# Kernel tuning notes

Measured on AMD Instinct MI355X. Metric: run time of the kernel, lower is better.

The kernel has to match this reference:

```python
import jax, jax.numpy as jnp
import numpy as np

N_ENT = 50000
N_USR = 10000
N_NODES = N_ENT + N_USR
D = 64            # entity_dim
AE_H = [128, 32]  # autoencoder hidden dims
CONV = [32, 16]   # graph conv output dims
R = 16            # n_relations
E = 1920000       # n_edges (avg degree 32)
B = 4096          # scoring batch


def setup_inputs() -> dict:
    key = jax.random.key(0)
    ks = jax.random.split(key, 24)
    s = 0.05
    rn = lambda k, shp: jax.random.normal(k, shp, jnp.float32) * s
    inp = {
        # int graph / batch inputs
        "users": jax.random.randint(ks[0], (B,), 0, N_USR),
        "items": jax.random.randint(ks[1], (B,), 0, N_ENT),
        "edge_src": jax.random.randint(ks[2], (E,), 0, N_NODES),
        "edge_dst": jax.random.randint(ks[3], (E,), 0, N_NODES),
        "edge_rel": jax.random.randint(ks[4], (E,), 0, R),
        # embeddings
        "entity_emb": rn(ks[5], (N_ENT, D)),
        "user_emb": rn(ks[6], (N_USR, D)),
        # autoencoder (weights stored [in, out])
        "enc_W0": rn(ks[7], (D, AE_H[0])), "enc_b0": jnp.zeros((AE_H[0],), jnp.float32),
        "enc_W1": rn(ks[8], (AE_H[0], AE_H[1])), "enc_b1": jnp.zeros((AE_H[1],), jnp.float32),
        "dec_W0": rn(ks[9], (AE_H[1], AE_H[0])), "dec_b0": jnp.zeros((AE_H[0],), jnp.float32),
        "dec_W1": rn(ks[10], (AE_H[0], D)), "dec_b1": jnp.zeros((D,), jnp.float32),
        # conv layer 1: input_dim=32 -> W_r [R, 64, 32], linear [64 -> 32]
        "Wr1": rn(ks[11], (R, 2 * CONV[0], CONV[0])),
        "lin_W1": rn(ks[12], (2 * CONV[0], CONV[0])), "lin_b1": jnp.zeros((CONV[0],), jnp.float32),
        # conv layer 2: input_dim=32 -> W_r [R, 64, 32], linear [64 -> 16]
        "Wr2": rn(ks[13], (R, 2 * CONV[0], CONV[0])),
        "lin_W2": rn(ks[14], (2 * CONV[0], CONV[1])), "lin_b2": jnp.zeros((CONV[1],), jnp.float32),
    }
    return inp


def _graph_conv(x, edge_src, edge_dst, edge_rel, W_r, lin_W, lin_b):
    # gate logit = sum_j (concat(h_dst, h_src) @ W_r[rel])_j
    #            = concat(h_dst, h_src) . W_r[rel].sum(-1)  (exact identity)
    w_sum = W_r.sum(axis=-1)                      # [R, 2*in]
    h_dst = x[edge_dst]                            # [E, in]
    h_src = x[edge_src]                            # [E, in]
    c = jnp.concatenate([h_dst, h_src], axis=-1)   # [E, 2*in]
    gate = jax.nn.sigmoid(jnp.sum(c * w_sum[edge_rel], axis=-1, keepdims=True))  # [E,1]
    weighted = h_src * gate                        # [E, in]
    n = x.shape[0]
    agg_sum = jax.ops.segment_sum(weighted, edge_dst, num_segments=n)           # [N, in]
    cnt = jax.ops.segment_sum(jnp.ones((edge_dst.shape[0], 1), x.dtype), edge_dst, num_segments=n)
    agg = jnp.where(cnt > 0, agg_sum / jnp.maximum(cnt, 1.0), 0.0)              # scatter-mean
    combined = jnp.concatenate([x, agg], axis=-1)  # [N, 2*in]
    return jax.nn.leaky_relu(combined @ lin_W + lin_b, negative_slope=0.01)


def reference(entity_emb, user_emb,
              enc_W0, enc_b0, enc_W1, enc_b1,
              dec_W0, dec_b0, dec_W1, dec_b1,
              Wr1, lin_W1, lin_b1, Wr2, lin_W2, lin_b2,
              users, items, edge_src, edge_dst, edge_rel):
    all_emb = jnp.concatenate([entity_emb, user_emb], axis=0)  # [N, 64]
    # autoencoder: ReLU between layers, none at the end of encode/decode
    encoded = jax.nn.relu(all_emb @ enc_W0 + enc_b0) @ enc_W1 + enc_b1  # [N, 32]
    decoded = jax.nn.relu(encoded @ dec_W0 + dec_b0) @ dec_W1 + dec_b1  # [N, 64]
    ae_loss = jnp.mean((decoded - all_emb) ** 2)

    x1 = _graph_conv(encoded, edge_src, edge_dst, edge_rel, Wr1, lin_W1, lin_b1)  # [N, 32]
    x2 = _graph_conv(x1, edge_src, edge_dst, edge_rel, Wr2, lin_W2, lin_b2)       # [N, 16]
    final = jnp.concatenate([x1, x2], axis=-1)  # [N, 48]

    user_nodes = N_ENT + users
    scores = jnp.sum(final[user_nodes] * final[items], axis=-1)  # [B]
    return scores, ae_loss
```

## Files before the change

### kernel.cpp

```cpp
#include <hip/hip_runtime.h>
#include <hip/hip_fp16.h>
#include <math.h>

#define N_ENT 50000
#define N_USR 10000
#define NN    60000
#define DD    64
#define H0    128
#define ENCD  32
#define RR    16
#define NB    256
#define BSH   8
#define NBU   235

__device__ __forceinline__ float4 ld4(const float* p){ return *reinterpret_cast<const float4*>(p); }
__device__ __forceinline__ void st4(float* p, float4 v){ *reinterpret_cast<float4*>(p) = v; }

__global__ __launch_bounds__(512, 6) void k_ae_hist(const float* __restrict__ ent, const float* __restrict__ usr,
    const float* __restrict__ eW0, const float* __restrict__ eb0,
    const float* __restrict__ eW1, const float* __restrict__ eb1,
    const float* __restrict__ dW0c, const float* __restrict__ db0,
    const float* __restrict__ dW1c, const float* __restrict__ db1,
    float* __restrict__ enc, float* __restrict__ loss_out,
    const int* __restrict__ edst, int* __restrict__ bktCnt,
    const float* __restrict__ Wr1, const float* __restrict__ Wr2, float* __restrict__ wsum,
    int E_, int nbAE, int nbTh){
  __shared__ float hs[H0][65];
  __shared__ float es[ENCD][65];
  __shared__ float sred[8];
  int bid = blockIdx.x;
  int t = threadIdx.x;

  if (bid >= nbAE){
    int rb = bid - nbAE;
    if (rb < nbTh){
      int* hh = (int*)&hs[0][0];
      if (t < NB) hh[t] = 0;
      __syncthreads();
      int i0 = rb*8192;
      #pragma unroll
      for (int k=0;k<16;k++){
        int e = i0 + k*512 + t;
        if (e < E_) atomicAdd(&hh[((unsigned)edst[e])>>BSH], 1);
      }
      __syncthreads();
      if (t < NB){ int c = hh[t]; if (c) atomicAdd(&bktCnt[t], c); }
    } else {
      int i = (rb - nbTh)*512 + t;
      if (i < 2*RR*DD){
        const float* Wr = (i < RR*DD) ? Wr1 : Wr2;
        int loc = i & (RR*DD - 1);
        const float* p = Wr + (size_t)loc*32;
        float s = 0.f;
        #pragma unroll
        for (int k=0;k<32;k++) s += p[k];
        wsum[i] = s;
      }
    }
    return;
  }

  int nl = t & 63;
  int wid = __builtin_amdgcn_readfirstlane(t >> 6);
  int gnode = bid*64 + nl;
  bool valid = gnode < NN;
  const float* xr = valid ? ((gnode < N_ENT) ? ent + (size_t)gnode*DD
                                             : usr + (size_t)(gnode-N_ENT)*DD)
                          : ent;

  {
    int j0 = wid*16;
    float acc[16];
    #pragma unroll
    for (int k=0;k<16;k++) acc[k]=eb0[j0+k];
    #pragma unroll
    for (int dc=0; dc<DD; dc+=16){
      float xv[16];
      #pragma unroll
      for (int q=0;q<4;q++){
        float4 v = ld4(xr + dc + 4*q);
        xv[4*q]=v.x; xv[4*q+1]=v.y; xv[4*q+2]=v.z; xv[4*q+3]=v.w;
      }
      #pragma unroll
      for (int dd=0; dd<16; dd++){
        const float* w = eW0 + (size_t)(dc+dd)*H0 + j0;
        #pragma unroll
        for (int k=0;k<16;k++) acc[k]=fmaf(xv[dd], w[k], acc[k]);
      }
    }
    #pragma unroll
    for (int k=0;k<16;k++) hs[j0+k][nl]=fmaxf(acc[k],0.f);
  }
  __syncthreads();

  {
    int k0 = wid*4;
    float acc[4];
    #pragma unroll
    for (int k=0;k<4;k++) acc[k]=eb1[k0+k];
    #pragma unroll 4
    for (int j=0;j<H0;j++){
      float hv = hs[j][nl];
      const float* w = eW1 + (size_t)j*ENCD + k0;
      #pragma unroll
      for (int k=0;k<4;k++) acc[k]=fmaf(hv,w[k],acc[k]);
    }
    #pragma unroll
    for (int k=0;k<4;k++) es[k0+k][nl]=acc[k];
  }
  __syncthreads();

  {
    int n2 = t >> 3;
    int k2 = (t & 7) * 4;
    int gn2 = bid*64 + n2;
    if (gn2 < NN){
      float4 a;
      a.x=es[k2+0][n2]; a.y=es[k2+1][n2]; a.z=es[k2+2][n2]; a.w=es[k2+3][n2];
      st4(enc + (size_t)gn2*ENCD + k2, a);
    }
  }

  {
    int j0 = wid*16;
    float acc[16];
    #pragma unroll
    for (int k=0;k<16;k++) acc[k]=db0[j0+k];
    #pragma unroll 4
    for (int d=0;d<ENCD;d++){
      float x = es[d][nl];
      const float* w = dW0c + (size_t)d*H0 + j0;
      #pragma unroll
      for (int k=0;k<16;k++) acc[k]=fmaf(x,w[k],acc[k]);
    }
    #pragma unroll
    for (int k=0;k<16;k++) hs[j0+k][nl]=fmaxf(acc[k],0.f);
  }
  __syncthreads();

  float part = 0.f;
  {
    int c0 = wid*8;
    float acc[8];
    #pragma unroll
    for (int k=0;k<8;k++) acc[k]=db1[c0+k];
    #pragma unroll 4
    for (int j=0;j<H0;j++){
      float hv = hs[j][nl];
      const float* w = dW1c + (size_t)j*DD + c0;
      #pragma unroll
      for (int k=0;k<8;k++) acc[k]=fmaf(hv,w[k],acc[k]);
    }
    if (valid){
      float xl[8];
      float4 v0 = ld4(xr + c0), v1 = ld4(xr + c0 + 4);
      xl[0]=v0.x; xl[1]=v0.y; xl[2]=v0.z; xl[3]=v0.w;
      xl[4]=v1.x; xl[5]=v1.y; xl[6]=v1.z; xl[7]=v1.w;
      #pragma unroll
      for (int k=0;k<8;k++){ float d_ = acc[k]-xl[k]; part = fmaf(d_,d_,part); }
    }
  }
  #pragma unroll
  for (int off=32; off>0; off>>=1) part += __shfl_down(part, off, 64);
  if ((t&63)==0) sred[wid] = part;
  __syncthreads();
  if (t==0){
    float s = 0.f;
    #pragma unroll
    for (int k=0;k<8;k++) s += sred[k];
    atomicAdd(loss_out, s * (1.0f/((float)NN*(float)DD)));
  }
}

__global__ __launch_bounds__(256) void k_scan256(const int* __restrict__ bktCnt, int* __restrict__ bktBase){
  __shared__ int wps[4];
  int t = threadIdx.x;
  int v = bktCnt[t];
  int x = v;
  #pragma unroll
  for (int off=1; off<64; off<<=1){
    int y = __shfl_up(x, off, 64);
    if ((t & 63) >= off) x += y;
  }
  if ((t & 63) == 63) wps[t >> 6] = x;
  __syncthreads();
  if (t < 4){
    int wv = wps[t];
    int wx = wv;
    #pragma unroll
    for (int off=1; off<4; off<<=1){
      int y = __shfl_up(wx, off, 4);
      if (t >= off) wx += y;
    }
    wps[t] = wx - wv;
  }
  __syncthreads();
  bktBase[t] = (x - v) + wps[t >> 6];
}

__global__ __launch_bounds__(256) void k_bucketA(const int* __restrict__ esrc, const int* __restrict__ edst,
    const int* __restrict__ erel, const int* __restrict__ bktBase, int* __restrict__ bktFill,
    unsigned* __restrict__ bktData, int E_){
  __shared__ int h[NB];
  __shared__ int gbase[NB];
  h[threadIdx.x]=0;
  __syncthreads();
  int i0 = blockIdx.x*4096;
  int dcache[16];
  #pragma unroll
  for (int k=0;k<16;k++){
    int e = i0 + k*256 + threadIdx.x;
    int d = (e < E_) ? edst[e] : -1;
    dcache[k] = d;
    if (d >= 0) atomicAdd(&h[((unsigned)d)>>BSH], 1);
  }
  __syncthreads();
  {
    int c = h[threadIdx.x];
    int off = c ? atomicAdd(&bktFill[threadIdx.x], c) : 0;
    gbase[threadIdx.x] = bktBase[threadIdx.x] + off;
    h[threadIdx.x] = 0;
  }
  __syncthreads();
  #pragma unroll
  for (int k=0;k<16;k++){
    int e = i0 + k*256 + threadIdx.x;
    if (e >= E_) continue;
    int d = dcache[k];
    int b = ((unsigned)d) >> BSH;
    int slot = atomicAdd(&h[b], 1);
    unsigned rec = (unsigned)esrc[e] | ((unsigned)erel[e] << 16) | ((unsigned)(d & 0xFF) << 20);
    bktData[(size_t)gbase[b] + slot] = rec;
  }
}

__global__ __launch_bounds__(256) void k_buildB(const unsigned* __restrict__ bktData,
    const int* __restrict__ bktBase, const int* __restrict__ bktCnt,
    int* __restrict__ rowp, int* __restrict__ packed){
  __shared__ int cnt[NB];
  __shared__ int start[NB];
  __shared__ int wps[4];
  int b = blockIdx.x;
  int base = bktBase[b];
  int n = bktCnt[b];
  int t = threadIdx.x;
  cnt[t] = 0;
  __syncthreads();
  for (int i=t; i<n; i+=256) atomicAdd(&cnt[(bktData[base+i] >> 20) & 0xFF], 1);
  __syncthreads();
  int v = cnt[t];
  cnt[t] = 0;
  int x = v;
  #pragma unroll
  for (int off=1; off<64; off<<=1){
    int y = __shfl_up(x, off, 64);
    if ((t & 63) >= off) x += y;
  }
  if ((t & 63) == 63) wps[t >> 6] = x;
  __syncthreads();
  if (t < 4){
    int wv = wps[t];
    int wx = wv;
    #pragma unroll
    for (int off=1; off<4; off<<=1){
      int y = __shfl_up(wx, off, 4);
      if (t >= off) wx += y;
    }
    wps[t] = wx - wv;
  }
  __syncthreads();
  int sv = (x - v) + wps[t >> 6];
  start[t] = sv;
  int node = (b << BSH) + t;
  if (node <= NN) rowp[node] = base + sv;
  __syncthreads();
  for (int i=t; i<n; i+=256){
    unsigned r = bktData[base+i];
    int dl = (r >> 20) & 0xFF;
    int p = start[dl] + atomicAdd(&cnt[dl], 1);
    packed[base + p] = (int)r;
  }
}

__global__ __launch_bounds__(256) void k_dots(const float* __restrict__ x, const float* __restrict__ wsum,
    float* __restrict__ dA, __half* __restrict__ dbrec, __half* __restrict__ xrec){
  __shared__ float wl[RR*DD];
  for (int i = threadIdx.x; i < RR*DD; i += 256){
    int r = i & 15; int j = i >> 4;
    wl[i] = wsum[r*DD + j];
  }
  __syncthreads();
  int t = blockIdx.x*256 + threadIdx.x;
  if (t >= NN*RR) return;
  int n = t >> 4, r = t & 15;
  const float* xr = x + (size_t)n*ENCD;
  float a = 0.f, b = 0.f;
  float xlo = 0.f, xhi = 0.f;
  #pragma unroll
  for (int q=0;q<8;q++){
    float4 v = ld4(xr + 4*q);
    int j = 4*q;
    if (r >= j && r < j+4){ float tmp[4]={v.x,v.y,v.z,v.w}; xlo = tmp[r-j]; }
    if (r+16 >= j && r+16 < j+4){ float tmp[4]={v.x,v.y,v.z,v.w}; xhi = tmp[r+16-j]; }
    a = fmaf(v.x, wl[(j+0)*16 + r], a);
    a = fmaf(v.y, wl[(j+1)*16 + r], a);
    a = fmaf(v.z, wl[(j+2)*16 + r], a);
    a = fmaf(v.w, wl[(j+3)*16 + r], a);
    b = fmaf(v.x, wl[(32+j+0)*16 + r], b);
    b = fmaf(v.y, wl[(32+j+1)*16 + r], b);
    b = fmaf(v.z, wl[(32+j+2)*16 + r], b);
    b = fmaf(v.w, wl[(32+j+3)*16 + r], b);
  }
  dA[t] = a;
  dbrec[t] = __float2half(b);
  xrec[(size_t)n*32 + r]      = __float2half(xlo);
  xrec[(size_t)n*32 + 16 + r] = __float2half(xhi);
}

__global__ __launch_bounds__(256) void k_gates(const int* __restrict__ packed,
    const int* __restrict__ bktBase, const int* __restrict__ bktCnt,
    const float* __restrict__ dA, const __half* __restrict__ dbrec, __half* __restrict__ gat){
  int b = blockIdx.x >> 2, g = blockIdx.x & 3;
  int base = bktBase[b], n = bktCnt[b];
  int lo = (n*g) >> 2, hi = (n*(g+1)) >> 2;
  for (int i = lo + (int)threadIdx.x; i < hi; i += 256){
    int p = packed[base+i];
    int s = p & 0xFFFF;
    int r = (p >> 16) & 15;
    int dl = (p >> 20) & 0xFF;
    int dst = (b << BSH) | dl;
    float z = dA[dst*16 + r] + __half2float(dbrec[s*16 + r]);
    gat[base+i] = __float2half(1.f/(1.f + __expf(-z)));
  }
}

__global__ __launch_bounds__(256) void k_agg(const __half2* __restrict__ xrec2, const int* __restrict__ packed,
    const __half* __restrict__ gat, const int* __restrict__ rowp, float* __restrict__ agg){
  int node = blockIdx.x*8 + (threadIdx.x >> 5);
  int l = threadIdx.x & 31;
  int half = l >> 4;
  int l16 = l & 15;
  if (node >= NN) return;
  int beg = rowp[node], end = rowp[node+1];
  float ax = 0.f, ay = 0.f;
  #pragma unroll 2
  for (int i = beg + half; i < end; i += 2){
    int p = packed[i];
    int s = p & 0xFFFF;
    float g = __half2float(gat[i]);
    float2 fx = __half22float2(xrec2[(size_t)s*16 + l16]);
    ax = fmaf(fx.x, g, ax);
    ay = fmaf(fx.y, g, ay);
  }
  ax += __shfl_xor(ax, 16, 32);
  ay += __shfl_xor(ay, 16, 32);
  if (half == 0){
    int deg = end - beg;
    float inv = (deg > 0) ? 1.f/(float)deg : 0.f;
    float2 o; o.x = ax*inv; o.y = ay*inv;
    *reinterpret_cast<float2*>(&agg[(size_t)node*ENCD + 2*l16]) = o;
  }
}

__global__ __launch_bounds__(256) void k_lin(const float* __restrict__ x, const float* __restrict__ agg,
    const float* __restrict__ W, const float* __restrict__ b, float* __restrict__ out, int outd){
  int n = blockIdx.x*256 + threadIdx.x;
  if (n >= NN) return;
  int k0 = blockIdx.y * 16;
  const float* xr = x   + (size_t)n*ENCD;
  const float* ar = agg + (size_t)n*ENCD;
  float xv[32], av[32];
  #pragma unroll
  for (int q=0;q<8;q++){ float4 v = ld4(xr+4*q); xv[4*q]=v.x; xv[4*q+1]=v.y; xv[4*q+2]=v.z; xv[4*q+3]=v.w; }
  #pragma unroll
  for (int q=0;q<8;q++){ float4 v = ld4(ar+4*q); av[4*q]=v.x; av[4*q+1]=v.y; av[4*q+2]=v.z; av[4*q+3]=v.w; }
  float acc[16];
  #pragma unroll
  for (int t=0;t<16;t++) acc[t] = b[k0+t];
  #pragma unroll
  for (int j=0;j<32;j++){
    #pragma unroll
    for (int t=0;t<16;t++) acc[t] = fmaf(xv[j], W[(size_t)j*outd + k0 + t], acc[t]);
  }
  #pragma unroll
  for (int j=0;j<32;j++){
    #pragma unroll
    for (int t=0;t<16;t++) acc[t] = fmaf(av[j], W[(size_t)(32+j)*outd + k0 + t], acc[t]);
  }
  float* o = out + (size_t)n*outd + k0;
  #pragma unroll
  for (int q=0;q<4;q++){
    float4 v;
    float a0=acc[4*q],a1=acc[4*q+1],a2=acc[4*q+2],a3=acc[4*q+3];
    v.x = a0>0.f? a0 : 0.01f*a0;
    v.y = a1>0.f? a1 : 0.01f*a1;
    v.z = a2>0.f? a2 : 0.01f*a2;
    v.w = a3>0.f? a3 : 0.01f*a3;
    st4(o + 4*q, v);
  }
}

__global__ __launch_bounds__(256) void k_score(const float* __restrict__ x1, const float* __restrict__ x2,
    const int* __restrict__ users, const int* __restrict__ items, float* __restrict__ out, int Bn){
  int b = blockIdx.x*256 + threadIdx.x;
  if (b >= Bn) return;
  int u  = N_ENT + users[b];
  int it = items[b];
  const float* a1 = x1 + (size_t)u*32;
  const float* c1 = x1 + (size_t)it*32;
  const float* a2 = x2 + (size_t)u*16;
  const float* c2 = x2 + (size_t)it*16;
  float s = 0.f;
  #pragma unroll
  for (int q=0;q<8;q++){
    float4 va=ld4(a1+4*q), vb=ld4(c1+4*q);
    s = fmaf(va.x,vb.x,s); s = fmaf(va.y,vb.y,s); s = fmaf(va.z,vb.z,s); s = fmaf(va.w,vb.w,s);
  }
  #pragma unroll
  for (int q=0;q<4;q++){
    float4 va=ld4(a2+4*q), vb=ld4(c2+4*q);
    s = fmaf(va.x,vb.x,s); s = fmaf(va.y,vb.y,s); s = fmaf(va.z,vb.z,s); s = fmaf(va.w,vb.w,s);
  }
  out[b] = s;
}

extern "C" void kernel_launch(void* const* d_in, const int* in_sizes, int n_in,
                              void* d_out, int out_size, void* d_ws, size_t ws_size,
                              hipStream_t stream){
  const int*   users   = (const int*)d_in[0];
  const int*   items   = (const int*)d_in[1];
  const int*   esrc    = (const int*)d_in[2];
  const int*   edst    = (const int*)d_in[3];
  const int*   erel    = (const int*)d_in[4];
  const float* ent     = (const float*)d_in[5];
  const float* usr     = (const float*)d_in[6];
  const float* enc_W0  = (const float*)d_in[7];
  const float* enc_b0  = (const float*)d_in[8];
  const float* enc_W1  = (const float*)d_in[9];
  const float* enc_b1  = (const float*)d_in[10];
  const float* dec_W0  = (const float*)d_in[11];
  const float* dec_b0  = (const float*)d_in[12];
  const float* dec_W1  = (const float*)d_in[13];
  const float* dec_b1  = (const float*)d_in[14];
  const float* Wr1     = (const float*)d_in[15];
  const float* lin_W1  = (const float*)d_in[16];
  const float* lin_b1  = (const float*)d_in[17];
  const float* Wr2     = (const float*)d_in[18];
  const float* lin_W2  = (const float*)d_in[19];
  const float* lin_b2  = (const float*)d_in[20];
  const int E = in_sizes[2];
  const int B = in_sizes[0];

  char* wp = (char*)d_ws;
  auto carve = [&](size_t bytes)->char*{ char* p = wp; wp += (bytes + 255) & ~(size_t)255; return p; };
  float* enc    = (float*)carve((size_t)NN*32*4);
  float* x1     = (float*)carve((size_t)NN*32*4);
  float* x2     = (float*)carve((size_t)NN*16*4);
  float* agg    = (float*)carve((size_t)NN*32*4);
  float* wsum   = (float*)carve((size_t)2*RR*DD*4);
  float* dA     = (float*)carve((size_t)NN*RR*4);
  __half* dbrec = (__half*)carve((size_t)NN*RR*2);
  __half* xrec  = (__half*)carve((size_t)NN*32*2);
  __half* gat   = (__half*)carve((size_t)E*2);
  int*   packed = (int*)  carve((size_t)E*4);
  unsigned* bktData = (unsigned*)carve((size_t)E*4);
  int*   bktCnt = (int*)  carve((size_t)2*NB*4);
  int*   bktFill= bktCnt + NB;
  int*   bktBase= (int*)  carve(NB*4);
  int*   rowp   = (int*)  carve(((size_t)NN+1)*4);

  const int nbN  = (NN + 255)/256;
  const int nbT  = (E + 4095)/4096;
  const int nbTh = (E + 8191)/8192;
  const int nbAE = (NN + 63)/64;
  const int nbD  = (NN*RR + 255)/256;
  dim3 blk(256);

  hipMemsetAsync(d_out, 0, (size_t)out_size*sizeof(float), stream);
  hipMemsetAsync(bktCnt, 0, (size_t)2*NB*sizeof(int), stream);

  k_ae_hist<<<dim3(nbAE + nbTh + 4), dim3(512), 0, stream>>>(
      ent, usr, enc_W0, enc_b0, enc_W1, enc_b1, dec_W0, dec_b0, dec_W1, dec_b1,
      enc, ((float*)d_out) + B, edst, bktCnt, Wr1, Wr2, wsum, E, nbAE, nbTh);

  k_scan256<<<1, blk, 0, stream>>>(bktCnt, bktBase);
  k_bucketA<<<nbT, blk, 0, stream>>>(esrc, edst, erel, bktBase, bktFill, bktData, E);
  k_buildB <<<NBU, blk, 0, stream>>>(bktData, bktBase, bktCnt, rowp, packed);

  k_dots <<<nbD, blk, 0, stream>>>(enc, wsum, dA, dbrec, xrec);
  k_gates<<<NBU*4, blk, 0, stream>>>(packed, bktBase, bktCnt, dA, dbrec, gat);
  k_agg  <<<(NN+7)/8, blk, 0, stream>>>((const __half2*)xrec, packed, gat, rowp, agg);
  k_lin  <<<dim3(nbN, 2), blk, 0, stream>>>(enc, agg, lin_W1, lin_b1, x1, 32);

  k_dots <<<nbD, blk, 0, stream>>>(x1, wsum + RR*DD, dA, dbrec, xrec);
  k_gates<<<NBU*4, blk, 0, stream>>>(packed, bktBase, bktCnt, dA, dbrec, gat);
  k_agg  <<<(NN+7)/8, blk, 0, stream>>>((const __half2*)xrec, packed, gat, rowp, agg);
  k_lin  <<<dim3(nbN, 1), blk, 0, stream>>>(x1, agg, lin_W2, lin_b2, x2, 16);

  k_score<<<(B+255)/256, blk, 0, stream>>>(x1, x2, users, items, (float*)d_out, B);
}
```

Baseline: 388.6 us.

## Fuse bucket scan into consumers, stage AE inputs in LDS, restructure aggregation

Measured after the change: 368.1 us. 5.3% less time.

```diff
diff --git a/kernel.cpp b/kernel.cpp
--- a/kernel.cpp
+++ b/kernel.cpp
@@ -25,16 +25,17 @@
     const int* __restrict__ edst, int* __restrict__ bktCnt,
     const float* __restrict__ Wr1, const float* __restrict__ Wr2, float* __restrict__ wsum,
     int E_, int nbAE, int nbTh){
-  __shared__ float hs[H0][65];
-  __shared__ float es[ENCD][65];
-  __shared__ float sred[8];
+  __shared__ float   xs[DD][65];
+  __shared__ __half2 hs2[H0/2][66];
+  __shared__ float   es[ENCD][65];
+  __shared__ float   sred[8];
   int bid = blockIdx.x;
   int t = threadIdx.x;
 
   if (bid >= nbAE){
     int rb = bid - nbAE;
     if (rb < nbTh){
-      int* hh = (int*)&hs[0][0];
+      int* hh = (int*)&xs[0][0];
       if (t < NB) hh[t] = 0;
       __syncthreads();
       int i0 = rb*8192;
@@ -62,34 +63,44 @@
 
   int nl = t & 63;
   int wid = __builtin_amdgcn_readfirstlane(t >> 6);
-  int gnode = bid*64 + nl;
-  bool valid = gnode < NN;
-  const float* xr = valid ? ((gnode < N_ENT) ? ent + (size_t)gnode*DD
-                                             : usr + (size_t)(gnode-N_ENT)*DD)
-                          : ent;
+
+  {
+    int n2 = t >> 3;
+    int d0 = (t & 7) * 8;
+    int gn = bid*64 + n2;
+    if (gn < NN){
+      const float* xr = (gn < N_ENT) ? ent + (size_t)gn*DD : usr + (size_t)(gn-N_ENT)*DD;
+      #pragma unroll
+      for (int q=0;q<2;q++){
+        float4 v = ld4(xr + d0 + 4*q);
+        xs[d0+4*q+0][n2]=v.x; xs[d0+4*q+1][n2]=v.y; xs[d0+4*q+2][n2]=v.z; xs[d0+4*q+3][n2]=v.w;
+      }
+    } else {
+      #pragma unroll
+      for (int q=0;q<8;q++) xs[d0+q][n2]=0.f;
+    }
+  }
+  __syncthreads();
 
   {
     int j0 = wid*16;
     float acc[16];
     #pragma unroll
     for (int k=0;k<16;k++) acc[k]=eb0[j0+k];
-    #pragma unroll
-    for (int dc=0; dc<DD; dc+=16){
-      float xv[16];
-      #pragma unroll
-      for (int q=0;q<4;q++){
-        float4 v = ld4(xr + dc + 4*q);
-        xv[4*q]=v.x; xv[4*q+1]=v.y; xv[4*q+2]=v.z; xv[4*q+3]=v.w;
-      }
-      #pragma unroll
-      for (int dd=0; dd<16; dd++){
-        const float* w = eW0 + (size_t)(dc+dd)*H0 + j0;
-        #pragma unroll
-        for (int k=0;k<16;k++) acc[k]=fmaf(xv[dd], w[k], acc[k]);
-      }
-    }
-    #pragma unroll
-    for (int k=0;k<16;k++) hs[j0+k][nl]=fmaxf(acc[k],0.f);
+    #pragma unroll 4
+    for (int d=0;d<DD;d++){
+      float x = xs[d][nl];
+      const float* w = eW0 + (size_t)d*H0 + j0;
+      #pragma unroll
+      for (int k=0;k<16;k++) acc[k]=fmaf(x,w[k],acc[k]);
+    }
+    #pragma unroll
+    for (int k=0;k<8;k++){
+      __half2 hv;
+      hv.x = __float2half(fmaxf(acc[2*k],0.f));
+      hv.y = __float2half(fmaxf(acc[2*k+1],0.f));
+      hs2[j0/2+k][nl] = hv;
+    }
   }
   __syncthreads();
 
@@ -99,11 +110,14 @@
     #pragma unroll
     for (int k=0;k<4;k++) acc[k]=eb1[k0+k];
     #pragma unroll 4
-    for (int j=0;j<H0;j++){
-      float hv = hs[j][nl];
-      const float* w = eW1 + (size_t)j*ENCD + k0;
-      #pragma unroll
-      for (int k=0;k<4;k++) acc[k]=fmaf(hv,w[k],acc[k]);
+    for (int jj=0;jj<H0/2;jj++){
+      float2 hv = __half22float2(hs2[jj][nl]);
+      const float* w0 = eW1 + (size_t)(2*jj)*ENCD + k0;
+      const float* w1 = w0 + ENCD;
+      #pragma unroll
+      for (int k=0;k<4;k++) acc[k]=fmaf(hv.x,w0[k],acc[k]);
+      #pragma unroll
+      for (int k=0;k<4;k++) acc[k]=fmaf(hv.y,w1[k],acc[k]);
     }
     #pragma unroll
     for (int k=0;k<4;k++) es[k0+k][nl]=acc[k];
@@ -134,7 +148,12 @@
       for (int k=0;k<16;k++) acc[k]=fmaf(x,w[k],acc[k]);
     }
     #pragma unroll
-    for (int k=0;k<16;k++) hs[j0+k][nl]=fmaxf(acc[k],0.f);
+    for (int k=0;k<8;k++){
+      __half2 hv;
+      hv.x = __float2half(fmaxf(acc[2*k],0.f));
+      hv.y = __float2half(fmaxf(acc[2*k+1],0.f));
+      hs2[j0/2+k][nl] = hv;
+    }
   }
   __syncthreads();
 
@@ -145,19 +164,19 @@
     #pragma unroll
     for (int k=0;k<8;k++) acc[k]=db1[c0+k];
     #pragma unroll 4
-    for (int j=0;j<H0;j++){
-      float hv = hs[j][nl];
-      const float* w = dW1c + (size_t)j*DD + c0;
-      #pragma unroll
-      for (int k=0;k<8;k++) acc[k]=fmaf(hv,w[k],acc[k]);
-    }
-    if (valid){
-      float xl[8];
-      float4 v0 = ld4(xr + c0), v1 = ld4(xr + c0 + 4);
-      xl[0]=v0.x; xl[1]=v0.y; xl[2]=v0.z; xl[3]=v0.w;
-      xl[4]=v1.x; xl[5]=v1.y; xl[6]=v1.z; xl[7]=v1.w;
-      #pragma unroll
-      for (int k=0;k<8;k++){ float d_ = acc[k]-xl[k]; part = fmaf(d_,d_,part); }
+    for (int jj=0;jj<H0/2;jj++){
+      float2 hv = __half22float2(hs2[jj][nl]);
+      const float* w0 = dW1c + (size_t)(2*jj)*DD + c0;
+      const float* w1 = w0 + DD;
+      #pragma unroll
+      for (int k=0;k<8;k++) acc[k]=fmaf(hv.x,w0[k],acc[k]);
+      #pragma unroll
+      for (int k=0;k<8;k++) acc[k]=fmaf(hv.y,w1[k],acc[k]);
+    }
+    int gnode = bid*64 + nl;
+    if (gnode < NN){
+      #pragma unroll
+      for (int k=0;k<8;k++){ float d_ = acc[k]-xs[c0+k][nl]; part = fmaf(d_,d_,part); }
     }
   }
   #pragma unroll
@@ -172,59 +191,49 @@
   }
 }
 
-__global__ __launch_bounds__(256) void k_scan256(const int* __restrict__ bktCnt, int* __restrict__ bktBase){
-  __shared__ int wps[4];
-  int t = threadIdx.x;
-  int v = bktCnt[t];
-  int x = v;
-  #pragma unroll
-  for (int off=1; off<64; off<<=1){
-    int y = __shfl_up(x, off, 64);
-    if ((t & 63) >= off) x += y;
-  }
-  if ((t & 63) == 63) wps[t >> 6] = x;
-  __syncthreads();
-  if (t < 4){
-    int wv = wps[t];
-    int wx = wv;
-    #pragma unroll
-    for (int off=1; off<4; off<<=1){
-      int y = __shfl_up(wx, off, 4);
-      if (t >= off) wx += y;
-    }
-    wps[t] = wx - wv;
-  }
-  __syncthreads();
-  bktBase[t] = (x - v) + wps[t >> 6];
-}
-
 __global__ __launch_bounds__(256) void k_bucketA(const int* __restrict__ esrc, const int* __restrict__ edst,
-    const int* __restrict__ erel, const int* __restrict__ bktBase, int* __restrict__ bktFill,
+    const int* __restrict__ erel, const int* __restrict__ bktCnt, int* __restrict__ bktFill,
     unsigned* __restrict__ bktData, int E_){
   __shared__ int h[NB];
   __shared__ int gbase[NB];
-  h[threadIdx.x]=0;
+  __shared__ int wps[4];
+  int t = threadIdx.x;
+  int cv = bktCnt[t];
+  int cx = cv;
+  #pragma unroll
+  for (int off=1; off<64; off<<=1){ int y=__shfl_up(cx,off,64); if ((t&63)>=off) cx+=y; }
+  if ((t&63)==63) wps[t>>6] = cx;
+  __syncthreads();
+  if (t<4){
+    int wv=wps[t]; int wx=wv;
+    #pragma unroll
+    for (int off=1; off<4; off<<=1){ int y=__shfl_up(wx,off,4); if (t>=off) wx+=y; }
+    wps[t]=wx-wv;
+  }
+  __syncthreads();
+  int sb = (cx - cv) + wps[t>>6];
+  h[t]=0;
   __syncthreads();
   int i0 = blockIdx.x*4096;
   int dcache[16];
   #pragma unroll
   for (int k=0;k<16;k++){
-    int e = i0 + k*256 + threadIdx.x;
+    int e = i0 + k*256 + t;
     int d = (e < E_) ? edst[e] : -1;
     dcache[k] = d;
     if (d >= 0) atomicAdd(&h[((unsigned)d)>>BSH], 1);
   }
   __syncthreads();
   {
-    int c = h[threadIdx.x];
-    int off = c ? atomicAdd(&bktFill[threadIdx.x], c) : 0;
-    gbase[threadIdx.x] = bktBase[threadIdx.x] + off;
-    h[threadIdx.x] = 0;
+    int c = h[t];
+    int off = c ? atomicAdd(&bktFill[t], c) : 0;
+    gbase[t] = sb + off;
+    h[t] = 0;
   }
   __syncthreads();
   #pragma unroll
   for (int k=0;k<16;k++){
-    int e = i0 + k*256 + threadIdx.x;
+    int e = i0 + k*256 + t;
     if (e >= E_) continue;
     int d = dcache[k];
     int b = ((unsigned)d) >> BSH;
@@ -235,50 +244,58 @@
 }
 
 __global__ __launch_bounds__(256) void k_buildB(const unsigned* __restrict__ bktData,
-    const int* __restrict__ bktBase, const int* __restrict__ bktCnt,
-    int* __restrict__ rowp, int* __restrict__ packed){
+    const int* __restrict__ bktCnt, int* __restrict__ rowp, int* __restrict__ packed){
   __shared__ int cnt[NB];
   __shared__ int start[NB];
   __shared__ int wps[4];
   int b = blockIdx.x;
-  int base = bktBase[b];
+  int t = threadIdx.x;
+  int cv = bktCnt[t];
+  int cx = cv;
+  #pragma unroll
+  for (int off=1; off<64; off<<=1){ int y=__shfl_up(cx,off,64); if ((t&63)>=off) cx+=y; }
+  if ((t&63)==63) wps[t>>6] = cx;
+  __syncthreads();
+  if (t<4){
+    int wv=wps[t]; int wx=wv;
+    #pragma unroll
+    for (int off=1; off<4; off<<=1){ int y=__shfl_up(wx,off,4); if (t>=off) wx+=y; }
+    wps[t]=wx-wv;
+  }
+  __syncthreads();
+  cnt[t] = (cx - cv) + wps[t>>6];
+  __syncthreads();
+  int base = cnt[b];
   int n = bktCnt[b];
-  int t = threadIdx.x;
+  __syncthreads();
   cnt[t] = 0;
   __syncthreads();
-  for (int i=t; i<n; i+=256) atomicAdd(&cnt[(bktData[base+i] >> 20) & 0xFF], 1);
+  for (int i=t; i<n; i+=256) atomicAdd(&cnt[(bktData[(size_t)base+i] >> 20) & 0xFF], 1);
   __syncthreads();
   int v = cnt[t];
   cnt[t] = 0;
   int x = v;
   #pragma unroll
-  for (int off=1; off<64; off<<=1){
-    int y = __shfl_up(x, off, 64);
-    if ((t & 63) >= off) x += y;
-  }
-  if ((t & 63) == 63) wps[t >> 6] = x;
-  __syncthreads();
-  if (t < 4){
-    int wv = wps[t];
-    int wx = wv;
-    #pragma unroll
-    for (int off=1; off<4; off<<=1){
-      int y = __shfl_up(wx, off, 4);
-      if (t >= off) wx += y;
-    }
-    wps[t] = wx - wv;
-  }
-  __syncthreads();
-  int sv = (x - v) + wps[t >> 6];
+  for (int off=1; off<64; off<<=1){ int y=__shfl_up(x,off,64); if ((t&63)>=off) x+=y; }
+  if ((t&63)==63) wps[t>>6] = x;
+  __syncthreads();
+  if (t<4){
+    int wv=wps[t]; int wx=wv;
+    #pragma unroll
+    for (int off=1; off<4; off<<=1){ int y=__shfl_up(wx,off,4); if (t>=off) wx+=y; }
+    wps[t]=wx-wv;
+  }
+  __syncthreads();
+  int sv = (x - v) + wps[t>>6];
   start[t] = sv;
   int node = (b << BSH) + t;
   if (node <= NN) rowp[node] = base + sv;
   __syncthreads();
   for (int i=t; i<n; i+=256){
-    unsigned r = bktData[base+i];
+    unsigned r = bktData[(size_t)base+i];
     int dl = (r >> 20) & 0xFF;
     int p = start[dl] + atomicAdd(&cnt[dl], 1);
-    packed[base + p] = (int)r;
+    packed[(size_t)base + p] = (int)r;
   }
 }
 
@@ -318,48 +335,57 @@
 }
 
 __global__ __launch_bounds__(256) void k_gates(const int* __restrict__ packed,
-    const int* __restrict__ bktBase, const int* __restrict__ bktCnt,
+    const int* __restrict__ bktBaseCnt, const int* __restrict__ bktCnt,
     const float* __restrict__ dA, const __half* __restrict__ dbrec, __half* __restrict__ gat){
   int b = blockIdx.x >> 2, g = blockIdx.x & 3;
-  int base = bktBase[b], n = bktCnt[b];
+  int base = bktBaseCnt[b << BSH];
+  int n = bktCnt[b];
   int lo = (n*g) >> 2, hi = (n*(g+1)) >> 2;
+  #pragma unroll 2
   for (int i = lo + (int)threadIdx.x; i < hi; i += 256){
-    int p = packed[base+i];
+    int p = packed[(size_t)base+i];
     int s = p & 0xFFFF;
     int r = (p >> 16) & 15;
     int dl = (p >> 20) & 0xFF;
     int dst = (b << BSH) | dl;
     float z = dA[dst*16 + r] + __half2float(dbrec[s*16 + r]);
-    gat[base+i] = __float2half(1.f/(1.f + __expf(-z)));
+    gat[(size_t)base+i] = __float2half(1.f/(1.f + __expf(-z)));
   }
 }
 
 __global__ __launch_bounds__(256) void k_agg(const __half2* __restrict__ xrec2, const int* __restrict__ packed,
     const __half* __restrict__ gat, const int* __restrict__ rowp, float* __restrict__ agg){
-  int node = blockIdx.x*8 + (threadIdx.x >> 5);
-  int l = threadIdx.x & 31;
-  int half = l >> 4;
-  int l16 = l & 15;
+  int node = blockIdx.x*16 + (threadIdx.x >> 4);
+  int l = threadIdx.x & 15;
   if (node >= NN) return;
   int beg = rowp[node], end = rowp[node+1];
   float ax = 0.f, ay = 0.f;
-  #pragma unroll 2
-  for (int i = beg + half; i < end; i += 2){
+  int i = beg;
+  for (; i + 4 <= end; i += 4){
+    int p0 = packed[i], p1 = packed[i+1], p2 = packed[i+2], p3 = packed[i+3];
+    float g0 = __half2float(gat[i]);
+    float g1 = __half2float(gat[i+1]);
+    float g2 = __half2float(gat[i+2]);
+    float g3 = __half2float(gat[i+3]);
+    float2 f0 = __half22float2(xrec2[(size_t)(p0 & 0xFFFF)*16 + l]);
+    float2 f1 = __half22float2(xrec2[(size_t)(p1 & 0xFFFF)*16 + l]);
+    float2 f2 = __half22float2(xrec2[(size_t)(p2 & 0xFFFF)*16 + l]);
+    float2 f3 = __half22float2(xrec2[(size_t)(p3 & 0xFFFF)*16 + l]);
+    ax = fmaf(f0.x, g0, ax); ay = fmaf(f0.y, g0, ay);
+    ax = fmaf(f1.x, g1, ax); ay = fmaf(f1.y, g1, ay);
+    ax = fmaf(f2.x, g2, ax); ay = fmaf(f2.y, g2, ay);
+    ax = fmaf(f3.x, g3, ax); ay = fmaf(f3.y, g3, ay);
+  }
+  for (; i < end; i++){
     int p = packed[i];
-    int s = p & 0xFFFF;
     float g = __half2float(gat[i]);
-    float2 fx = __half22float2(xrec2[(size_t)s*16 + l16]);
-    ax = fmaf(fx.x, g, ax);
-    ay = fmaf(fx.y, g, ay);
-  }
-  ax += __shfl_xor(ax, 16, 32);
-  ay += __shfl_xor(ay, 16, 32);
-  if (half == 0){
-    int deg = end - beg;
-    float inv = (deg > 0) ? 1.f/(float)deg : 0.f;
-    float2 o; o.x = ax*inv; o.y = ay*inv;
-    *reinterpret_cast<float2*>(&agg[(size_t)node*ENCD + 2*l16]) = o;
-  }
+    float2 fx = __half22float2(xrec2[(size_t)(p & 0xFFFF)*16 + l]);
+    ax = fmaf(fx.x, g, ax); ay = fmaf(fx.y, g, ay);
+  }
+  int deg = end - beg;
+  float inv = (deg > 0) ? 1.f/(float)deg : 0.f;
+  float2 o; o.x = ax*inv; o.y = ay*inv;
+  *reinterpret_cast<float2*>(&agg[(size_t)node*ENCD + 2*l]) = o;
 }
 
 __global__ __launch_bounds__(256) void k_lin(const float* __restrict__ x, const float* __restrict__ agg,
@@ -466,8 +492,7 @@
   unsigned* bktData = (unsigned*)carve((size_t)E*4);
   int*   bktCnt = (int*)  carve((size_t)2*NB*4);
   int*   bktFill= bktCnt + NB;
-  int*   bktBase= (int*)  carve(NB*4);
-  int*   rowp   = (int*)  carve(((size_t)NN+1)*4);
+  int*   rowp   = (int*)  carve(((size_t)NN+256)*4);
 
   const int nbN  = (NN + 255)/256;
   const int nbT  = (E + 4095)/4096;
@@ -483,18 +508,17 @@
       ent, usr, enc_W0, enc_b0, enc_W1, enc_b1, dec_W0, dec_b0, dec_W1, dec_b1,
       enc, ((float*)d_out) + B, edst, bktCnt, Wr1, Wr2, wsum, E, nbAE, nbTh);
 
-  k_scan256<<<1, blk, 0, stream>>>(bktCnt, bktBase);
-  k_bucketA<<<nbT, blk, 0, stream>>>(esrc, edst, erel, bktBase, bktFill, bktData, E);
-  k_buildB <<<NBU, blk, 0, stream>>>(bktData, bktBase, bktCnt, rowp, packed);
+  k_bucketA<<<nbT, blk, 0, stream>>>(esrc, edst, erel, bktCnt, bktFill, bktData, E);
+  k_buildB <<<NBU, blk, 0, stream>>>(bktData, bktCnt, rowp, packed);
 
   k_dots <<<nbD, blk, 0, stream>>>(enc, wsum, dA, dbrec, xrec);
-  k_gates<<<NBU*4, blk, 0, stream>>>(packed, bktBase, bktCnt, dA, dbrec, gat);
-  k_agg  <<<(NN+7)/8, blk, 0, stream>>>((const __half2*)xrec, packed, gat, rowp, agg);
+  k_gates<<<NBU*4, blk, 0, stream>>>(packed, rowp, bktCnt, dA, dbrec, gat);
+  k_agg  <<<(NN+15)/16, blk, 0, stream>>>((const __half2*)xrec, packed, gat, rowp, agg);
   k_lin  <<<dim3(nbN, 2), blk, 0, stream>>>(enc, agg, lin_W1, lin_b1, x1, 32);
 
   k_dots <<<nbD, blk, 0, stream>>>(x1, wsum + RR*DD, dA, dbrec, xrec);
-  k_gates<<<NBU*4, blk, 0, stream>>>(packed, bktBase, bktCnt, dA, dbrec, gat);
-  k_agg  <<<(NN+7)/8, blk, 0, stream>>>((const __half2*)xrec, packed, gat, rowp, agg);
+  k_gates<<<NBU*4, blk, 0, stream>>>(packed, rowp, bktCnt, dA, dbrec, gat);
+  k_agg  <<<(NN+15)/16, blk, 0, stream>>>((const __half2*)xrec, packed, gat, rowp, agg);
   k_lin  <<<dim3(nbN, 1), blk, 0, stream>>>(x1, agg, lin_W2, lin_b2, x2, 16);
 
   k_score<<<(B+255)/256, blk, 0, stream>>>(x1, x2, users, items, (float*)d_out, B);
```
